# Kernel tuning notes

Hardware: AMD Instinct MI355X
Metric: run time of the kernel (lower is better)

The kernel has to match this reference:

```python
import jax, jax.numpy as jnp
import numpy as np

NUM_Q = 4
BETA = 0.25
TEMP = 0.1
EPS = 1e-12


def setup_inputs() -> dict:
    key = jax.random.key(0)
    k1, k2, k3, k4 = jax.random.split(key, 4)
    N, D, NE, K = 32768, 256, 256, 4096
    return {
        "x": jax.random.normal(k1, (N, D), dtype=jnp.float32),
        "codebooks": jax.random.normal(k2, (NUM_Q, NE, D), dtype=jnp.float32) * 0.02,
        "pair_idx1": jax.random.randint(k3, (K,), 0, N),
        "pair_idx2": jax.random.randint(k4, (K,), 0, N),
    }


def _quantize(residual, codebook):
    # squared L2 cdist: ||r||^2 - 2 r.e + ||e||^2  -> [N, n_e]
    d2 = (jnp.sum(residual * residual, axis=1, keepdims=True)
          - 2.0 * residual @ codebook.T
          + jnp.sum(codebook * codebook, axis=1))
    idx = jnp.argmin(d2, axis=1)                      # [N]
    q = codebook[idx]                                 # gather [N, D]
    sg = jax.lax.stop_gradient
    loss = jnp.mean((sg(q) - residual) ** 2) + BETA * jnp.mean((q - sg(residual)) ** 2)
    x_res = residual + sg(q - residual)               # straight-through
    return x_res, loss, idx


def _outer_contrastive(feat, i1, i2):
    # L2-normalize rows (torch F.normalize, eps clamp)
    xn = feat * jax.lax.rsqrt(jnp.sum(feat * feat, axis=1, keepdims=True) + EPS)
    pos = jnp.sum(xn[i1] * xn[i2], axis=1) / TEMP     # [K]
    sim = (xn[i1] @ xn.T) / TEMP                      # [K, N]
    # CE with positive at sim[:, i2]; excluded-positive column equals pos,
    # so logsumexp over [pos, negatives] == logsumexp over the full row.
    return jnp.mean(jax.nn.logsumexp(sim, axis=1) - pos)


def reference(x, codebooks, pair_idx1, pair_idx2):
    residual = x
    x_q = jnp.zeros_like(x)
    vq_losses, outer_losses, all_idx = [], [], []
    for q in range(NUM_Q):
        outer_losses.append(_outer_contrastive(residual, pair_idx1, pair_idx2))
        x_res, loss, idx = _quantize(residual, codebooks[q])
        residual = residual - x_res
        x_q = x_q + x_res
        vq_losses.append(loss)
        all_idx.append(idx)
    mean_loss = jnp.mean(jnp.stack(vq_losses))
    return (x_q, mean_loss, jnp.stack(outer_losses), jnp.stack(all_idx, axis=-1))
```

## Files before the change

kernel.cpp:

```cpp
#include <hip/hip_runtime.h>

#define N_ROWS 32768
#define DIM    256
#define NE     256
#define KP     4096
#define NQ     4
#define ND     8388608
#define RESCORE_MARGIN 2e-4f

typedef short short8 __attribute__((ext_vector_type(8)));
typedef unsigned short ushort8v __attribute__((ext_vector_type(8)));
typedef float f32x4  __attribute__((ext_vector_type(4)));

__device__ inline float bf2f(unsigned short u) {
  return __uint_as_float(((unsigned)u) << 16);
}
__device__ inline unsigned short f2bf(float f) {
  unsigned u = __float_as_uint(f);
  u += 0x7fffu + ((u >> 16) & 1u);
  return (unsigned short)(u >> 16);
}

__device__ inline size_t chunkIdx(int row, int j) {
  return (size_t)(((row >> 4) * 8 + (j >> 2)) * 64 + ((j & 3) << 4) + (row & 15));
}

__global__ __launch_bounds__(256) void prep0_kernel(
    const float* __restrict__ x,
    unsigned short* __restrict__ Xnp, float* __restrict__ rnorm,
    unsigned short* __restrict__ rHp, unsigned short* __restrict__ rLp) {
  const int tid = threadIdx.x, wave = tid >> 6, lane = tid & 63;
  const int half = lane >> 5, j = lane & 31;
  const int row = blockIdx.x * 8 + wave * 2 + half;
  const float4* xr = (const float4*)(x + (size_t)row * DIM + j * 8);
  float4 v0 = xr[0], v1 = xr[1];
  float vv[8] = {v0.x, v0.y, v0.z, v0.w, v1.x, v1.y, v1.z, v1.w};
  float ss = 0.f;
#pragma unroll
  for (int i = 0; i < 8; ++i) ss += vv[i] * vv[i];
#pragma unroll
  for (int m = 1; m < 32; m <<= 1) ss += __shfl_xor(ss, m, 64);
  if (j == 0) rnorm[row] = ss;
  const float sc = rsqrtf(ss + 1e-12f);
  ushort8v h, l, xn;
#pragma unroll
  for (int i = 0; i < 8; ++i) {
    h[i] = f2bf(vv[i]); l[i] = f2bf(vv[i] - bf2f(h[i])); xn[i] = f2bf(vv[i] * sc);
  }
  const size_t c = chunkIdx(row, j) * 8;
  *(ushort8v*)(rHp + c) = h;
  *(ushort8v*)(rLp + c) = l;
  *(ushort8v*)(Xnp + c) = xn;
}

__global__ __launch_bounds__(256) void cbnorm_kernel(
    const float* __restrict__ cb, float* __restrict__ cbn) {
  const int wave = threadIdx.x >> 6, lane = threadIdx.x & 63;
  const int e = blockIdx.x * 4 + wave;
  float4 v = ((const float4*)(cb + (size_t)e * DIM))[lane];
  float ss = v.x * v.x + v.y * v.y + v.z * v.z + v.w * v.w;
#pragma unroll
  for (int m = 1; m < 64; m <<= 1) ss += __shfl_xor(ss, m, 64);
  if (lane == 0) cbn[e] = ss;
}

__global__ __launch_bounds__(256) void cbsplit_kernel(
    const float* __restrict__ cb, unsigned short* __restrict__ cbHp,
    unsigned short* __restrict__ cbLp) {
  const int p = blockIdx.x * 256 + threadIdx.x;
  const int stage = p >> 13, ps = p & 8191;
  const int l16 = ps & 15, quad = (ps >> 4) & 3, kf = (ps >> 6) & 7, et = ps >> 9;
  const int e = et * 16 + l16, k0 = kf * 32 + quad * 8;
  const float* src = cb + ((size_t)(stage * NE + e)) * DIM + k0;
  float4 v0 = ((const float4*)src)[0], v1 = ((const float4*)src)[1];
  float vv[8] = {v0.x, v0.y, v0.z, v0.w, v1.x, v1.y, v1.z, v1.w};
  ushort8v h, l;
#pragma unroll
  for (int i = 0; i < 8; ++i) {
    h[i] = f2bf(vv[i]); l[i] = f2bf(vv[i] - bf2f(h[i]));
  }
  *(ushort8v*)(cbHp + (size_t)p * 8) = h;
  *(ushort8v*)(cbLp + (size_t)p * 8) = l;
}

__global__ __launch_bounds__(256) void gather_pos_kernel(
    const unsigned short* __restrict__ Xnp, const int* __restrict__ i1,
    const int* __restrict__ i2, unsigned short* __restrict__ Qgp,
    float* __restrict__ pos, float* __restrict__ ssum) {
  if (blockIdx.x < 16) ssum[blockIdx.x * 256 + threadIdx.x] = 0.0f;
  const int wave = threadIdx.x >> 6, lane = threadIdx.x & 63;
  const int k = blockIdx.x * 4 + wave;
  const int a = i1[k], b = i2[k];
  const int j2 = lane >> 1, off = (lane & 1) * 4;
  ushort4 va = *(const ushort4*)(Xnp + chunkIdx(a, j2) * 8 + off);
  ushort4 vb = *(const ushort4*)(Xnp + chunkIdx(b, j2) * 8 + off);
  *(ushort4*)(Qgp + chunkIdx(k, j2) * 8 + off) = va;
  float d = bf2f(va.x) * bf2f(vb.x) + bf2f(va.y) * bf2f(vb.y) +
            bf2f(va.z) * bf2f(vb.z) + bf2f(va.w) * bf2f(vb.w);
#pragma unroll
  for (int m = 1; m < 64; m <<= 1) d += __shfl_xor(d, m, 64);
  if (lane == 0) pos[k] = d * 10.0f;
}

__global__ __launch_bounds__(256, 2) void sim_lse_kernel(
    const unsigned short* __restrict__ Qgp, const unsigned short* __restrict__ Xnp,
    float* __restrict__ s_sum) {
  __shared__ unsigned short ldsB[4096];
  const int tid  = threadIdx.x;
  const int lane = tid & 63;
  const int wave = tid >> 6;
  const int quad = lane >> 4;
  const int l16  = lane & 15;

  const int fid = blockIdx.y * 32 + blockIdx.x;
  const int xcd = fid & 7;
  const int sl  = fid >> 3;
  const int bx  = sl & 31;
  const int by  = xcd * 8 + (sl >> 5);

  const int qt0  = bx * 8 + wave * 2;
  const int qbase = bx * 128 + wave * 32;

  short8 a[2][8];
#pragma unroll
  for (int t = 0; t < 2; ++t)
#pragma unroll
    for (int f = 0; f < 8; ++f)
      a[t][f] = *(const short8*)(Qgp + ((size_t)(((qt0 + t) * 8 + f) * 64 + lane)) * 8);

  float s[2][4] = {};
  const float C1 = 14.4269504088896341f;
  const unsigned short* bsrc = Xnp + (size_t)(by * 32) * 4096;

  auto stageB = [&](int g) {
    const unsigned short* src = bsrc + (size_t)g * 4096 + wave * 1024 + lane * 8;
#pragma unroll
    for (int p = 0; p < 2; ++p)
      __builtin_amdgcn_global_load_lds(
          (const __attribute__((address_space(1))) unsigned int*)(src + p * 512),
          (__attribute__((address_space(3))) unsigned int*)(&ldsB[wave * 1024 + p * 512]),
          16, 0, 0);
  };

  stageB(0);
  for (int g = 0; g < 32; ++g) {
    asm volatile("s_waitcnt vmcnt(0)" ::: "memory");
    __builtin_amdgcn_s_barrier();
    __builtin_amdgcn_sched_barrier(0);
    short8 b[8];
#pragma unroll
    for (int f = 0; f < 8; ++f)
      b[f] = *(const short8*)(&ldsB[f * 512 + lane * 8]);
    asm volatile("s_waitcnt lgkmcnt(0)" ::: "memory");
    __builtin_amdgcn_s_barrier();
    __builtin_amdgcn_sched_barrier(0);
    if (g + 1 < 32) stageB(g + 1);

    f32x4 acc0[2] = {{0.f, 0.f, 0.f, 0.f}, {0.f, 0.f, 0.f, 0.f}};
    f32x4 acc1[2] = {{0.f, 0.f, 0.f, 0.f}, {0.f, 0.f, 0.f, 0.f}};
#pragma unroll
    for (int f = 0; f < 4; ++f)
#pragma unroll
      for (int t = 0; t < 2; ++t) {
        acc0[t] = __builtin_amdgcn_mfma_f32_16x16x32_bf16(a[t][f], b[f], acc0[t], 0, 0, 0);
        acc1[t] = __builtin_amdgcn_mfma_f32_16x16x32_bf16(a[t][f + 4], b[f + 4], acc1[t], 0, 0, 0);
      }
#pragma unroll
    for (int t = 0; t < 2; ++t) {
      f32x4 m = acc0[t] + acc1[t];
#pragma unroll
      for (int i = 0; i < 4; ++i)
        s[t][i] += exp2f(fmaf(m[i], C1, -C1));
    }
  }
#pragma unroll
  for (int m = 1; m < 16; m <<= 1)
#pragma unroll
    for (int t = 0; t < 2; ++t)
#pragma unroll
      for (int i = 0; i < 4; ++i) s[t][i] += __shfl_xor(s[t][i], m, 64);
  if (l16 == 0) {
#pragma unroll
    for (int t = 0; t < 2; ++t)
#pragma unroll
      for (int i = 0; i < 4; ++i)
        atomicAdd(&s_sum[qbase + t * 16 + quad * 4 + i], s[t][i]);
  }
}

__global__ __launch_bounds__(256) void lse_final_kernel(
    const float* __restrict__ s_sum, const float* __restrict__ pos,
    float* __restrict__ acc, int stage) {
  const int t = threadIdx.x;
  const int k = blockIdx.x * 256 + t;
  float v = 10.0f + __logf(s_sum[k]) - pos[k];
#pragma unroll
  for (int m = 1; m < 64; m <<= 1) v += __shfl_xor(v, m, 64);
  __shared__ float red[4];
  if ((t & 63) == 0) red[t >> 6] = v;
  __syncthreads();
  if (t == 0) atomicAdd(&acc[4 + stage], red[0] + red[1] + red[2] + red[3]);
}

__global__ __launch_bounds__(256, 2) void argmin_update_kernel(
    const float* __restrict__ xin, float* __restrict__ resid,
    const float* __restrict__ cb,
    const unsigned short* __restrict__ cbHp, const unsigned short* __restrict__ cbLp,
    const float* __restrict__ cbn, float* __restrict__ rnorm,
    unsigned short* rHp, unsigned short* rLp,
    float* __restrict__ xq, float* __restrict__ idxf, float* __restrict__ acc,
    unsigned short* __restrict__ Xnp, int stage) {
  __shared__ float sV1[4][32];
  __shared__ float sV2[4][32];
  __shared__ int   sIx[4][32];
  __shared__ int   sIdx[32];
  __shared__ int   sFlag[32];
  __shared__ float sred[4];
  const int tid  = threadIdx.x;
  const int lane = tid & 63;
  const int wave = tid >> 6;
  const int quad = lane >> 4;
  const int l16  = lane & 15;
  const int rbase = blockIdx.x * 32;
  const int t0 = blockIdx.x * 2;
  const float* __restrict__ src = (stage == 0) ? xin : resid;

  f32x4 acc4[2][4];
#pragma unroll
  for (int rt = 0; rt < 2; ++rt)
#pragma unroll
    for (int ct = 0; ct < 4; ++ct) acc4[rt][ct] = (f32x4){0.f, 0.f, 0.f, 0.f};

  auto loadA = [&](int kf, short8 (&aH)[2], short8 (&aL)[2]) {
#pragma unroll
    for (int rt = 0; rt < 2; ++rt) {
      const size_t off = ((size_t)(((t0 + rt) * 8 + kf) * 64 + lane)) * 8;
      aH[rt] = *(const short8*)(rHp + off);
      aL[rt] = *(const short8*)(rLp + off);
    }
  };
  auto loadBc = [&](int kf, short8 (&bH)[4], short8 (&bL)[4]) {
#pragma unroll
    for (int ct = 0; ct < 4; ++ct) {
      const size_t boff = ((size_t)(((wave * 4 + ct) * 8 + kf) * 64 + lane)) * 8;
      bH[ct] = *(const short8*)(cbHp + boff);
      bL[ct] = *(const short8*)(cbLp + boff);
    }
  };
  auto computeK = [&](short8 (&aH)[2], short8 (&aL)[2], short8 (&bH)[4],
                      short8 (&bL)[4]) {
#pragma unroll
    for (int ct = 0; ct < 4; ++ct)
#pragma unroll
      for (int rt = 0; rt < 2; ++rt) {
        acc4[rt][ct] = __builtin_amdgcn_mfma_f32_16x16x32_bf16(aL[rt], bH[ct], acc4[rt][ct], 0, 0, 0);
        acc4[rt][ct] = __builtin_amdgcn_mfma_f32_16x16x32_bf16(aH[rt], bL[ct], acc4[rt][ct], 0, 0, 0);
        acc4[rt][ct] = __builtin_amdgcn_mfma_f32_16x16x32_bf16(aH[rt], bH[ct], acc4[rt][ct], 0, 0, 0);
      }
  };

  short8 aH0[2], aL0[2], bH0[4], bL0[4], aH1[2], aL1[2], bH1[4], bL1[4];
  loadA(0, aH0, aL0); loadBc(0, bH0, bL0);
  for (int kf = 0; kf < 8; kf += 2) {
    loadA(kf + 1, aH1, aL1); loadBc(kf + 1, bH1, bL1);
    computeK(aH0, aL0, bH0, bL0);
    if (kf + 2 < 8) { loadA(kf + 2, aH0, aL0); loadBc(kf + 2, bH0, bL0); }
    computeK(aH1, aL1, bH1, bL1);
  }

  float cbe[4];
#pragma unroll
  for (int ct = 0; ct < 4; ++ct) cbe[ct] = cbn[(wave * 4 + ct) * 16 + l16];
#pragma unroll
  for (int rt = 0; rt < 2; ++rt) {
    float b1[4], b2[4]; int e1[4];
#pragma unroll
    for (int i = 0; i < 4; ++i) { b1[i] = 3.4e38f; b2[i] = 3.4e38f; e1[i] = 0; }
#pragma unroll
    for (int ct = 0; ct < 4; ++ct) {
      const int e = (wave * 4 + ct) * 16 + l16;
#pragma unroll
      for (int i = 0; i < 4; ++i) {
        const float v = fmaf(-2.0f, acc4[rt][ct][i], cbe[ct]);
        if (v < b1[i]) { b2[i] = b1[i]; b1[i] = v; e1[i] = e; }
        else if (v < b2[i]) b2[i] = v;
      }
    }
#pragma unroll
    for (int m = 1; m < 16; m <<= 1) {
#pragma unroll
      for (int i = 0; i < 4; ++i) {
        const float o1 = __shfl_xor(b1[i], m, 64);
        const float o2 = __shfl_xor(b2[i], m, 64);
        const int   oe = __shfl_xor(e1[i], m, 64);
        if (o1 < b1[i] || (o1 == b1[i] && oe < e1[i])) {
          b2[i] = fminf(b1[i], o2); b1[i] = o1; e1[i] = oe;
        } else {
          b2[i] = fminf(b2[i], o1);
        }
      }
    }
    if (l16 == 0) {
#pragma unroll
      for (int i = 0; i < 4; ++i) {
        const int r = rt * 16 + quad * 4 + i;
        sV1[wave][r] = b1[i]; sV2[wave][r] = b2[i]; sIx[wave][r] = e1[i];
      }
    }
  }
  __syncthreads();
  if (tid < 32) {
    float v1 = 3.4e38f, v2 = 3.4e38f; int ix = 0;
#pragma unroll
    for (int w = 0; w < 4; ++w) {
      const float a1 = sV1[w][tid], a2 = sV2[w][tid];
      const int ae = sIx[w][tid];
      if (a1 < v1) { v2 = fminf(v1, a2); v1 = a1; ix = ae; }
      else { v2 = fminf(v2, fminf(a1, a2)); }
    }
    sIdx[tid] = ix;
    sFlag[tid] = (v2 - v1 < RESCORE_MARGIN) ? 1 : 0;
  }
  __syncthreads();

  for (int rr = 0; rr < 8; ++rr) {
    const int r = wave * 8 + rr;
    if (sFlag[r]) {
      const int row = rbase + r;
      const float* rrow = src + (size_t)row * DIM;
      float d[4] = {0.f, 0.f, 0.f, 0.f};
      for (int kb = 0; kb < 64; ++kb) {
        const float4 rv = ((const float4*)rrow)[kb];
#pragma unroll
        for (int j = 0; j < 4; ++j) {
          const float4 cv = ((const float4*)(cb + (size_t)(lane + 64 * j) * DIM))[kb];
          d[j] = fmaf(rv.x, cv.x, d[j]);
          d[j] = fmaf(rv.y, cv.y, d[j]);
          d[j] = fmaf(rv.z, cv.z, d[j]);
          d[j] = fmaf(rv.w, cv.w, d[j]);
        }
      }
      const float rn = rnorm[row];
      float bv = 3.4e38f; int be = 0;
#pragma unroll
      for (int j = 0; j < 4; ++j) {
        const int e = lane + 64 * j;
        const float v = (rn - 2.0f * d[j]) + cbn[e];
        if (v < bv) { bv = v; be = e; }
      }
#pragma unroll
      for (int m = 1; m < 64; m <<= 1) {
        const float vo = __shfl_xor(bv, m, 64);
        const int   eo = __shfl_xor(be, m, 64);
        if (vo < bv || (vo == bv && eo < be)) { bv = vo; be = eo; }
      }
      if (lane == 0) sIdx[r] = be;
    }
  }
  __syncthreads();

  const int half = lane >> 5, j = lane & 31;
  float msum = 0.0f;
  for (int i = 0; i < 4; ++i) {
    const int rr = i * 8 + wave * 2 + half;
    const int row = rbase + rr;
    const int e = sIdx[rr];
    const float4* rp = (const float4*)(src + (size_t)row * DIM + j * 8);
    float4 r0 = rp[0], r1 = rp[1];
    const float4* qp = (const float4*)(cb + (size_t)e * DIM + j * 8);
    float4 q0 = qp[0], q1 = qp[1];
    float nr[8] = {r0.x - q0.x, r0.y - q0.y, r0.z - q0.z, r0.w - q0.w,
                   r1.x - q1.x, r1.y - q1.y, r1.z - q1.z, r1.w - q1.w};
    float ss = 0.f;
#pragma unroll
    for (int u = 0; u < 8; ++u) ss += nr[u] * nr[u];
    if (stage == 3) {
      const float4* xr = (const float4*)(xin + (size_t)row * DIM + j * 8);
      float4 x0 = xr[0], x1 = xr[1];
      float4* xp = (float4*)(xq + (size_t)row * DIM + j * 8);
      xp[0] = (float4){x0.x - nr[0], x0.y - nr[1], x0.z - nr[2], x0.w - nr[3]};
      xp[1] = (float4){x1.x - nr[4], x1.y - nr[5], x1.z - nr[6], x1.w - nr[7]};
    }
#pragma unroll
    for (int m = 1; m < 32; m <<= 1) ss += __shfl_xor(ss, m, 64);
    if (stage < 3) {
      float4* rw = (float4*)(resid + (size_t)row * DIM + j * 8);
      rw[0] = (float4){nr[0], nr[1], nr[2], nr[3]};
      rw[1] = (float4){nr[4], nr[5], nr[6], nr[7]};
      const float sc = rsqrtf(ss + 1e-12f);
      ushort8v h, l, xn;
#pragma unroll
      for (int u = 0; u < 8; ++u) {
        h[u] = f2bf(nr[u]); l[u] = f2bf(nr[u] - bf2f(h[u])); xn[u] = f2bf(nr[u] * sc);
      }
      const size_t c = chunkIdx(row, j) * 8;
      *(ushort8v*)(rHp + c) = h;
      *(ushort8v*)(rLp + c) = l;
      *(ushort8v*)(Xnp + c) = xn;
      if (j == 0) rnorm[row] = ss;
    }
    if (j == 0) {
      idxf[(size_t)row * NQ + stage] = (float)e;
      msum += ss;
    }
  }
  msum += __shfl_xor(msum, 32, 64);
  if (lane == 0) sred[wave] = msum;
  __syncthreads();
  if (tid == 0) atomicAdd(&acc[0], sred[0] + sred[1] + sred[2] + sred[3]);
}

__global__ void finalize_kernel(const float* __restrict__ acc, float* __restrict__ out) {
  const int t = threadIdx.x;
  if (t == 0) out[ND] = acc[0] * (1.25f / (4.0f * (float)ND));
  if (t < 4) out[ND + 1 + t] = acc[4 + t] * (1.0f / (float)KP);
}

extern "C" void kernel_launch(void* const* d_in, const int* in_sizes, int n_in,
                              void* d_out, int out_size, void* d_ws, size_t ws_size,
                              hipStream_t stream) {
  const float* x         = (const float*)d_in[0];
  const float* codebooks = (const float*)d_in[1];
  const int*   i1        = (const int*)d_in[2];
  const int*   i2        = (const int*)d_in[3];
  float* out = (float*)d_out;
  float* out_xq   = out;
  float* out_idxf = out + ND + 1 + NQ;

  char* w = (char*)d_ws;
  float*          resid = (float*)w;          w += (size_t)N_ROWS * DIM * 4;
  unsigned short* Xnp   = (unsigned short*)w; w += (size_t)N_ROWS * DIM * 2;
  unsigned short* rHp   = (unsigned short*)w; w += (size_t)N_ROWS * DIM * 2;
  unsigned short* rLp   = (unsigned short*)w; w += (size_t)N_ROWS * DIM * 2;
  float*          rnorm = (float*)w;          w += (size_t)N_ROWS * 4;
  unsigned short* Qgp   = (unsigned short*)w; w += (size_t)KP * DIM * 2;
  float*          pos   = (float*)w;          w += (size_t)KP * 4;
  float*          ssum  = (float*)w;          w += (size_t)KP * 4;
  float*          cbn   = (float*)w;          w += (size_t)NQ * NE * 4;
  unsigned short* cbHp  = (unsigned short*)w; w += (size_t)NQ * NE * DIM * 2;
  unsigned short* cbLp  = (unsigned short*)w; w += (size_t)NQ * NE * DIM * 2;
  float*          acc   = (float*)w;          w += 32;

  prep0_kernel<<<4096, 256, 0, stream>>>(x, Xnp, rnorm, rHp, rLp);
  cbnorm_kernel<<<256, 256, 0, stream>>>(codebooks, cbn);
  cbsplit_kernel<<<128, 256, 0, stream>>>(codebooks, cbHp, cbLp);
  hipMemsetAsync(acc, 0, 32, stream);
  for (int q = 0; q < NQ; ++q) {
    const float* cb = codebooks + (size_t)q * NE * DIM;
    gather_pos_kernel<<<1024, 256, 0, stream>>>(Xnp, i1, i2, Qgp, pos, ssum);
    sim_lse_kernel<<<dim3(32, 64), 256, 0, stream>>>(Qgp, Xnp, ssum);
    lse_final_kernel<<<16, 256, 0, stream>>>(ssum, pos, acc, q);
    argmin_update_kernel<<<1024, 256, 0, stream>>>(
        x, resid, cb, cbHp + (size_t)q * NE * DIM, cbLp + (size_t)q * NE * DIM,
        cbn + q * NE, rnorm, rHp, rLp, out_xq, out_idxf, acc, Xnp, q);
  }
  finalize_kernel<<<1, 64, 0, stream>>>(acc, out);
}
```

Before: 656.5 us.

## Use 32x32x16 MFMA with double-buffered LDS tiles in similarity LSE kernel

Rewrites the contrastive sim/logsumexp kernel to use 32x32x16 bf16 MFMA instead of 16x16x32, with each wave computing a 32x32 tile per step. The B tile in LDS is now double-buffered and each stage holds twice as many rows, so the next global-to-LDS load is issued before the current buffer is read and one barrier per iteration is dropped. The aim is fewer MFMA instructions and better overlap of loads with compute. In exchange it uses four times the LDS, more registers for the 16-wide accumulators, and depends on a changed operand indexing that must match the packed layout.

```diff
diff --git a/kernel.cpp b/kernel.cpp
--- a/kernel.cpp
+++ b/kernel.cpp
@@ -11,6 +11,7 @@
 typedef short short8 __attribute__((ext_vector_type(8)));
 typedef unsigned short ushort8v __attribute__((ext_vector_type(8)));
 typedef float f32x4  __attribute__((ext_vector_type(4)));
+typedef float f32x16 __attribute__((ext_vector_type(16)));
 
 __device__ inline float bf2f(unsigned short u) {
   return __uint_as_float(((unsigned)u) << 16);
@@ -105,12 +106,12 @@
 __global__ __launch_bounds__(256, 2) void sim_lse_kernel(
     const unsigned short* __restrict__ Qgp, const unsigned short* __restrict__ Xnp,
     float* __restrict__ s_sum) {
-  __shared__ unsigned short ldsB[4096];
+  __shared__ unsigned short ldsB[16384];
   const int tid  = threadIdx.x;
   const int lane = tid & 63;
   const int wave = tid >> 6;
-  const int quad = lane >> 4;
-  const int l16  = lane & 15;
+  const int r32  = lane & 31;
+  const int h    = lane >> 5;
 
   const int fid = blockIdx.y * 32 + blockIdx.x;
   const int xcd = fid & 7;
@@ -118,73 +119,71 @@
   const int bx  = sl & 31;
   const int by  = xcd * 8 + (sl >> 5);
 
-  const int qt0  = bx * 8 + wave * 2;
   const int qbase = bx * 128 + wave * 32;
 
-  short8 a[2][8];
-#pragma unroll
-  for (int t = 0; t < 2; ++t)
-#pragma unroll
-    for (int f = 0; f < 8; ++f)
-      a[t][f] = *(const short8*)(Qgp + ((size_t)(((qt0 + t) * 8 + f) * 64 + lane)) * 8);
-
-  float s[2][4] = {};
+  const unsigned short* abase =
+      Qgp + (size_t)(bx * 8 + wave * 2 + (r32 >> 4)) * 4096 + h * 128 + (r32 & 15) * 8;
+  short8 a[16];
+#pragma unroll
+  for (int f = 0; f < 16; ++f) a[f] = *(const short8*)(abase + f * 256);
+
+  float s[16];
+#pragma unroll
+  for (int i = 0; i < 16; ++i) s[i] = 0.f;
+  const f32x16 z16 = {0.f, 0.f, 0.f, 0.f, 0.f, 0.f, 0.f, 0.f,
+                      0.f, 0.f, 0.f, 0.f, 0.f, 0.f, 0.f, 0.f};
   const float C1 = 14.4269504088896341f;
-  const unsigned short* bsrc = Xnp + (size_t)(by * 32) * 4096;
-
-  auto stageB = [&](int g) {
-    const unsigned short* src = bsrc + (size_t)g * 4096 + wave * 1024 + lane * 8;
-#pragma unroll
-    for (int p = 0; p < 2; ++p)
+
+  const int lbase = (r32 >> 4) * 8192 + h * 256 + (r32 & 15) * 16;
+
+  auto stageB = [&](int g, int pp) {
+    const unsigned short* sp =
+        Xnp + (size_t)(by * 32 + g * 2) * 4096 + wave * 512 + lane * 8;
+    unsigned short* dp = &ldsB[pp * 8192 + wave * 512 + lane * 8];
+#pragma unroll
+    for (int p = 0; p < 4; ++p)
       __builtin_amdgcn_global_load_lds(
-          (const __attribute__((address_space(1))) unsigned int*)(src + p * 512),
-          (__attribute__((address_space(3))) unsigned int*)(&ldsB[wave * 1024 + p * 512]),
+          (const __attribute__((address_space(1))) unsigned int*)(sp + p * 2048),
+          (__attribute__((address_space(3))) unsigned int*)(dp + p * 2048),
           16, 0, 0);
   };
 
-  stageB(0);
-  for (int g = 0; g < 32; ++g) {
+  stageB(0, 0);
+  for (int g = 0; g < 16; ++g) {
+    const int pp = g & 1;
     asm volatile("s_waitcnt vmcnt(0)" ::: "memory");
     __builtin_amdgcn_s_barrier();
     __builtin_amdgcn_sched_barrier(0);
-    short8 b[8];
-#pragma unroll
-    for (int f = 0; f < 8; ++f)
-      b[f] = *(const short8*)(&ldsB[f * 512 + lane * 8]);
-    asm volatile("s_waitcnt lgkmcnt(0)" ::: "memory");
-    __builtin_amdgcn_s_barrier();
-    __builtin_amdgcn_sched_barrier(0);
-    if (g + 1 < 32) stageB(g + 1);
-
-    f32x4 acc0[2] = {{0.f, 0.f, 0.f, 0.f}, {0.f, 0.f, 0.f, 0.f}};
-    f32x4 acc1[2] = {{0.f, 0.f, 0.f, 0.f}, {0.f, 0.f, 0.f, 0.f}};
-#pragma unroll
-    for (int f = 0; f < 4; ++f)
-#pragma unroll
-      for (int t = 0; t < 2; ++t) {
-        acc0[t] = __builtin_amdgcn_mfma_f32_16x16x32_bf16(a[t][f], b[f], acc0[t], 0, 0, 0);
-        acc1[t] = __builtin_amdgcn_mfma_f32_16x16x32_bf16(a[t][f + 4], b[f + 4], acc1[t], 0, 0, 0);
-      }
-#pragma unroll
-    for (int t = 0; t < 2; ++t) {
-      f32x4 m = acc0[t] + acc1[t];
-#pragma unroll
-      for (int i = 0; i < 4; ++i)
-        s[t][i] += exp2f(fmaf(m[i], C1, -C1));
-    }
-  }
-#pragma unroll
-  for (int m = 1; m < 16; m <<= 1)
-#pragma unroll
-    for (int t = 0; t < 2; ++t)
-#pragma unroll
-      for (int i = 0; i < 4; ++i) s[t][i] += __shfl_xor(s[t][i], m, 64);
-  if (l16 == 0) {
-#pragma unroll
-    for (int t = 0; t < 2; ++t)
-#pragma unroll
-      for (int i = 0; i < 4; ++i)
-        atomicAdd(&s_sum[qbase + t * 16 + quad * 4 + i], s[t][i]);
+    if (g + 1 < 16) stageB(g + 1, pp ^ 1);
+
+    const char* bufR = (const char*)&ldsB[pp * 8192];
+    short8 b[16];
+#pragma unroll
+    for (int f = 0; f < 16; ++f)
+      b[f] = *(const short8*)(bufR + lbase + f * 512);
+
+    f32x16 accA = __builtin_amdgcn_mfma_f32_32x32x16_bf16(a[0], b[0], z16, 0, 0, 0);
+    f32x16 accB = __builtin_amdgcn_mfma_f32_32x32x16_bf16(a[8], b[8], z16, 0, 0, 0);
+#pragma unroll
+    for (int f = 1; f < 8; ++f) {
+      accA = __builtin_amdgcn_mfma_f32_32x32x16_bf16(a[f], b[f], accA, 0, 0, 0);
+      accB = __builtin_amdgcn_mfma_f32_32x32x16_bf16(a[f + 8], b[f + 8], accB, 0, 0, 0);
+    }
+#pragma unroll
+    for (int i = 0; i < 16; ++i)
+      s[i] += exp2f(fmaf(accA[i] + accB[i], C1, -C1));
+  }
+
+#pragma unroll
+  for (int m = 1; m < 32; m <<= 1)
+#pragma unroll
+    for (int i = 0; i < 16; ++i) s[i] += __shfl_xor(s[i], m, 64);
+  if (r32 == 0) {
+#pragma unroll
+    for (int i = 0; i < 16; ++i) {
+      const int row = (i & 3) + 8 * (i >> 2) + 4 * h;
+      atomicAdd(&s_sum[qbase + row], s[i]);
+    }
   }
 }
 
```

Result: slower. 672.1 us (+2.4%).
